# Optimization experiments

Measured on AMD Instinct MI355X. Metric: run time of the kernel, lower is better.

## Reference

```python
import jax, jax.numpy as jnp
import numpy as np

NH = 16      # num_heads
D = 128      # head_dim
C = 64       # chunk_size
EPS = 1e-12  # F.normalize eps


def setup_inputs() -> dict:
    key = jax.random.key(0)
    ks = jax.random.split(key, 12)
    B, L, H = 4, 4096, 2048
    std = 0.02
    f32 = jnp.float32
    inp = {
        "hidden_states": jax.random.normal(ks[0], (B, L, H), f32),
        # torch nn.Linear weights are [out_features, in_features]
        "q_w": jax.random.normal(ks[1], (NH * D, H), f32) * std,
        "q_b": jnp.zeros((NH * D,), f32),
        "k_w": jax.random.normal(ks[2], (NH * D, H), f32) * std,
        "k_b": jnp.zeros((NH * D,), f32),
        "v_w": jax.random.normal(ks[3], (NH * D, H), f32) * std,
        "v_b": jnp.zeros((NH * D,), f32),
        "a_w": jax.random.normal(ks[4], (NH, H), f32) * std,
        "a_b": jnp.zeros((NH,), f32),
        "b_w": jax.random.normal(ks[5], (NH, H), f32) * std,
        "b_b": jnp.zeros((NH,), f32),
        "og_w": jax.random.normal(ks[6], (NH * D, H), f32) * std,  # no bias
        "o_w": jax.random.normal(ks[7], (H, NH * D), f32) * std,
        "o_b": jnp.zeros((H,), f32),
    }
    return inp


def _l2norm(x):
    n = jnp.linalg.norm(x, axis=-1, keepdims=True)
    return x / jnp.maximum(n, EPS)


def reference(hidden_states, q_w, q_b, k_w, k_b, v_w, v_b,
              a_w, a_b, b_w, b_b, og_w, o_w, o_b):
    B, L, H = hidden_states.shape
    nh, d, c = NH, D, C
    hs = hidden_states

    q = (hs @ q_w.T + q_b).reshape(B, L, nh, d)
    k = (hs @ k_w.T + k_b).reshape(B, L, nh, d)
    v = (hs @ v_w.T + v_b).reshape(B, L, nh, d)
    # alpha = sigmoid(hs @ a_w.T + a_b) is computed in the original module but
    # never affects the output (alpha_mean / log_alpha are dead code) -> omitted.
    beta = jax.nn.softplus(hs @ b_w.T + b_b)            # [B,L,nh]

    scale = float(d) ** 0.5
    qn = _l2norm(q / scale)                              # normalize makes /scale moot, kept faithful
    kn = _l2norm(k / scale)
    gv = beta[..., None] * v                             # [B,L,nh,d]

    nchunks = L // c

    def to_chunks(x):  # [B,L,nh,d] -> [B,nchunks,nh,c,d]
        return x.reshape(B, nchunks, c, nh, d).transpose(0, 1, 3, 2, 4)

    qc, kc, gvc = to_chunks(qn), to_chunks(kn), to_chunks(gv)

    attn = jnp.einsum('bnhid,bnhjd->bnhij', qc, kc)      # per-chunk QK^T
    pos = jnp.arange(c, dtype=jnp.float32)
    dist = jnp.clip(pos[None, :] - pos[:, None], 0.0, None)   # (j-i) clamped >=0
    decay = jnp.exp(-0.1 * dist)
    causal = pos[None, :] <= pos[:, None]                # keep j<=i, zero j>i
    mask = jnp.where(causal, decay, 0.0)                 # [c,c]
    out = jnp.einsum('bnhij,bnhjd->bnhid', attn * mask, gvc)

    out = out.transpose(0, 1, 3, 2, 4).reshape(B, L, nh * d)
    gate = jax.nn.silu(hs @ og_w.T)                      # output_gate has no bias
    out = out * gate
    return out @ o_w.T + o_b
```

## Files before the change

kernel.cpp:

```cpp
#include <hip/hip_runtime.h>


typedef __bf16 bf16x8 __attribute__((ext_vector_type(8)));
typedef float f32x4 __attribute__((ext_vector_type(4)));

typedef __attribute__((address_space(1))) const unsigned int g_u32;
typedef __attribute__((address_space(3))) unsigned int l_u32;

__device__ __forceinline__ void cp16(const unsigned short* g, unsigned short* l) {
  __builtin_amdgcn_global_load_lds((g_u32*)g, (l_u32*)l, 16, 0, 0);
}

__device__ __forceinline__ unsigned short f2bf(float x) {
  unsigned u = __builtin_bit_cast(unsigned, x);
  u += 0x7fffu + ((u >> 16) & 1u);
  return (unsigned short)(u >> 16);
}
__device__ __forceinline__ float bf2f(unsigned short h) {
  return __builtin_bit_cast(float, (unsigned)h << 16);
}
__device__ __forceinline__ unsigned pk2(float a, float b) {
  return (unsigned)f2bf(a) | ((unsigned)f2bf(b) << 16);
}

__global__ __launch_bounds__(256) void cvt_bf16(const float* __restrict__ in,
                                                unsigned short* __restrict__ out,
                                                int n) {
  int i = (blockIdx.x * 256 + threadIdx.x) * 8;
  if (i >= n) return;
  float4 f0 = *(const float4*)(in + i);
  float4 f1 = *(const float4*)(in + i + 4);
  uint4 u;
  u.x = pk2(f0.x, f0.y); u.y = pk2(f0.z, f0.w);
  u.z = pk2(f1.x, f1.y); u.w = pk2(f1.z, f1.w);
  *(uint4*)(out + i) = u;
}

__global__ __launch_bounds__(256) void build_bias(
    const float* __restrict__ qb, const float* __restrict__ kb,
    const float* __restrict__ vb, float* __restrict__ bias_cat) {
  int i = blockIdx.x * 256 + threadIdx.x;
  float v = 0.f;
  if (i < 2048) v = qb[i];
  else if (i < 4096) v = kb[i - 2048];
  else if (i < 6144) v = vb[i - 4096];
  bias_cat[i] = v;
}

__global__ __launch_bounds__(256) void beta_kernel(
    const float* __restrict__ hs, const float* __restrict__ bw,
    const float* __restrict__ bb, float* __restrict__ beta,
    unsigned short* __restrict__ hsb) {
  __shared__ float row[2048];
  __shared__ float part[16][17];
  const int m = blockIdx.x;
  const float* src = hs + (size_t)m * 2048;
  for (int i = threadIdx.x; i < 512; i += 256)
    ((float4*)row)[i] = ((const float4*)src)[i];
  __syncthreads();
  if (hsb) {
    int e = threadIdx.x * 8;
    uint4 u;
    u.x = pk2(row[e], row[e + 1]);     u.y = pk2(row[e + 2], row[e + 3]);
    u.z = pk2(row[e + 4], row[e + 5]); u.w = pk2(row[e + 6], row[e + 7]);
    *(uint4*)(hsb + (size_t)m * 2048 + e) = u;
  }
  const int h = threadIdx.x >> 4, j = threadIdx.x & 15;
  const float* w = bw + h * 2048;
  float s = 0.f;
  #pragma unroll 8
  for (int kk = 0; kk < 128; kk++) {
    int k = j + (kk << 4);
    s += row[k] * w[k];
  }
  part[h][j] = s;
  __syncthreads();
  if (threadIdx.x < 16) {
    int hh = threadIdx.x;
    float t = bb[hh];
    #pragma unroll
    for (int j2 = 0; j2 < 16; j2++) t += part[hh][j2];
    beta[(size_t)m * 16 + hh] = fmaxf(t, 0.f) + log1pf(__expf(-fabsf(t)));
  }
}

template <int EPI, int N, int K>
__global__ __launch_bounds__(512, 2) void gemm256(
    const unsigned short* __restrict__ A, const unsigned short* __restrict__ Bw,
    const float* __restrict__ bias, const float* __restrict__ beta,
    void* __restrict__ Cv) {
  constexpr int NT = K / 64;
  static_assert(NT >= 3, "pipeline needs >=3 K-steps");
  __shared__ __align__(16) unsigned short S[2 * 32768];
  const int tid = threadIdx.x;
  const int m0 = blockIdx.y * 256;
  const int n0 = blockIdx.x * 256;
  const int wid = tid >> 6, lane = tid & 63;
  const int wm = wid >> 2, wn = wid & 3;
  const int quad = lane >> 4, l16 = lane & 15;

  const int sidx = tid >> 3;
  const int sc = tid & 7;
  const int scol = ((sc ^ (sidx & 7)) << 3);
  const unsigned short* pA = A + (size_t)(m0 + sidx) * K + scol;
  const int rbx = ((sidx >> 5) << 6) + (sidx & 31);
  const unsigned short* pB = Bw + (size_t)(n0 + rbx) * K + scol;

  auto STG = [&](int roff , const unsigned short* src) {
    cp16(src, S + roff + tid * 8);
    cp16(src + (size_t)128 * K, S + roff + 4096 + tid * 8);
  };

  const int sig = l16 & 7;
  const int ck0 = ((quad ^ sig) << 4);
  const int ck1 = (((4 + quad) ^ sig) << 4);
  const int aro = (wm * 64 + l16) * 128;
  const int bro = (wn * 32 + l16) * 128;

  f32x4 acc[8][4] = {};
  bf16x8 aL[4][2], aH[4][2], bX[2][2], bY[2][2];

  STG(0,             pA);
  STG(8192,          pA + (size_t)64 * K);
  STG(16384,         pB);
  STG(24576,         pB + (size_t)32 * K);
  STG(32768,         pA + 64);
  STG(32768 + 16384, pB + 64);
  STG(32768 + 24576, pB + (size_t)32 * K + 64);
  asm volatile("s_waitcnt vmcnt(6)" ::: "memory");
  __builtin_amdgcn_s_barrier();

  for (int t = 0; t < NT; ++t) {
    const int cur = (t & 1) << 15;
    const int nxt = 32768 - cur;
    const char* B0 = (const char*)S + cur * 2;
    const int koff1 = (t + 1 < NT ? t + 1 : NT - 1) * 64;
    const int koff2 = (t + 2 < NT ? t + 2 : NT - 1) * 64;

    #pragma unroll
    for (int mi = 0; mi < 4; mi++) {
      aL[mi][0] = *(const bf16x8*)(B0 + aro + mi * 2048 + ck0);
      aL[mi][1] = *(const bf16x8*)(B0 + aro + mi * 2048 + ck1);
    }
    #pragma unroll
    for (int ni = 0; ni < 2; ni++) {
      bX[ni][0] = *(const bf16x8*)(B0 + 32768 + bro + ni * 2048 + ck0);
      bX[ni][1] = *(const bf16x8*)(B0 + 32768 + bro + ni * 2048 + ck1);
    }
    STG(nxt + 8192, pA + (size_t)64 * K + koff1);
    __builtin_amdgcn_s_barrier();
    __builtin_amdgcn_s_setprio(1);
    #pragma unroll
    for (int k = 0; k < 2; k++)
      #pragma unroll
      for (int mi = 0; mi < 4; mi++)
        #pragma unroll
        for (int ni = 0; ni < 2; ni++)
          acc[mi][ni] = __builtin_amdgcn_mfma_f32_16x16x32_bf16(
              aL[mi][k], bX[ni][k], acc[mi][ni], 0, 0, 0);
    __builtin_amdgcn_s_setprio(0);
    __builtin_amdgcn_s_barrier();

    #pragma unroll
    for (int ni = 0; ni < 2; ni++) {
      bY[ni][0] = *(const bf16x8*)(B0 + 49152 + bro + ni * 2048 + ck0);
      bY[ni][1] = *(const bf16x8*)(B0 + 49152 + bro + ni * 2048 + ck1);
    }
    STG(cur, pA + koff2);
    __builtin_amdgcn_s_barrier();
    __builtin_amdgcn_s_setprio(1);
    #pragma unroll
    for (int k = 0; k < 2; k++)
      #pragma unroll
      for (int mi = 0; mi < 4; mi++)
        #pragma unroll
        for (int ni = 0; ni < 2; ni++)
          acc[mi][2 + ni] = __builtin_amdgcn_mfma_f32_16x16x32_bf16(
              aL[mi][k], bY[ni][k], acc[mi][2 + ni], 0, 0, 0);
    __builtin_amdgcn_s_setprio(0);
    __builtin_amdgcn_s_barrier();

    #pragma unroll
    for (int mi = 0; mi < 4; mi++) {
      aH[mi][0] = *(const bf16x8*)(B0 + 16384 + aro + mi * 2048 + ck0);
      aH[mi][1] = *(const bf16x8*)(B0 + 16384 + aro + mi * 2048 + ck1);
    }
    STG(cur + 16384, pB + koff2);
    __builtin_amdgcn_s_barrier();
    __builtin_amdgcn_s_setprio(1);
    #pragma unroll
    for (int k = 0; k < 2; k++)
      #pragma unroll
      for (int mi = 0; mi < 4; mi++)
        #pragma unroll
        for (int ni = 0; ni < 2; ni++)
          acc[4 + mi][2 + ni] = __builtin_amdgcn_mfma_f32_16x16x32_bf16(
              aH[mi][k], bY[ni][k], acc[4 + mi][2 + ni], 0, 0, 0);
    __builtin_amdgcn_s_setprio(0);
    __builtin_amdgcn_s_barrier();

    STG(cur + 24576, pB + (size_t)32 * K + koff2);
    __builtin_amdgcn_s_setprio(1);
    #pragma unroll
    for (int k = 0; k < 2; k++)
      #pragma unroll
      for (int mi = 0; mi < 4; mi++)
        #pragma unroll
        for (int ni = 0; ni < 2; ni++)
          acc[4 + mi][ni] = __builtin_amdgcn_mfma_f32_16x16x32_bf16(
              aH[mi][k], bX[ni][k], acc[4 + mi][ni], 0, 0, 0);
    __builtin_amdgcn_s_setprio(0);
    asm volatile("s_waitcnt vmcnt(6)" ::: "memory");
    __builtin_amdgcn_s_barrier();
  }
  asm volatile("s_waitcnt vmcnt(0)" ::: "memory");

  if (EPI == 0) {
    const int mode = n0 >> 11;
    unsigned short* outp =
        (unsigned short*)Cv + (size_t)mode * ((size_t)16384 * 2048);
    const int head = ((n0 + wn * 64) >> 7) & 15;
    #pragma unroll
    for (int mi = 0; mi < 8; mi++) {
      #pragma unroll
      for (int r = 0; r < 4; r++) {
        const int row = m0 + wm * 128 + mi * 16 + quad * 4 + r;
        const float bsc = (mode == 2) ? beta[(size_t)row * 16 + head] : 1.f;
        #pragma unroll
        for (int ni = 0; ni < 4; ni++) {
          const int col = n0 + wn * 64 + ni * 16 + l16;
          float x = acc[mi][ni][r] + bias[col];
          if (mode == 2) x *= bsc;
          if (mode == 3) x = x / (1.f + __expf(-x));
          outp[(size_t)row * 2048 + (col & 2047)] = f2bf(x);
        }
      }
    }
  } else {
    #pragma unroll
    for (int mi = 0; mi < 8; mi++)
      #pragma unroll
      for (int r = 0; r < 4; r++) {
        const int row = m0 + wm * 128 + mi * 16 + quad * 4 + r;
        #pragma unroll
        for (int ni = 0; ni < 4; ni++) {
          const int col = n0 + wn * 64 + ni * 16 + l16;
          ((float*)Cv)[(size_t)row * N + col] = acc[mi][ni][r] + bias[col];
        }
      }
  }
}

constexpr int GLDW = 40;
template <int EPI, bool ABF16>
__global__ __launch_bounds__(256) void gemm_bt(
    const void* __restrict__ Av, const float* __restrict__ Bw,
    const float* __restrict__ bias, const float* __restrict__ beta,
    void* __restrict__ Cv, int M, int N, int K) {
  __shared__ unsigned short As[128 * GLDW];
  __shared__ unsigned short Bs[128 * GLDW];
  const int tid = threadIdx.x;
  const int m0 = blockIdx.y * 128;
  const int n0 = blockIdx.x * 128;
  const int wid = tid >> 6, lane = tid & 63;
  const int wm = wid >> 1, wn = wid & 1;
  const int quad = lane >> 4, l16 = lane & 15;
  const int srow = tid >> 1, skh = (tid & 1) << 4;

  f32x4 acc[4][4] = {};
  const float* Bg = Bw + (size_t)(n0 + srow) * K + skh;

  for (int kb = 0; kb < K; kb += 32) {
    if (ABF16) {
      const unsigned short* Ag =
          (const unsigned short*)Av + (size_t)(m0 + srow) * K + kb + skh;
      uint4 u0 = ((const uint4*)Ag)[0];
      uint4 u1 = ((const uint4*)Ag)[1];
      uint4* d = (uint4*)&As[srow * GLDW + skh];
      d[0] = u0; d[1] = u1;
    } else {
      const float* Ag = (const float*)Av + (size_t)(m0 + srow) * K + kb + skh;
      float4 f0 = ((const float4*)Ag)[0];
      float4 f1 = ((const float4*)Ag)[1];
      float4 f2 = ((const float4*)Ag)[2];
      float4 f3 = ((const float4*)Ag)[3];
      unsigned* d = (unsigned*)&As[srow * GLDW + skh];
      d[0] = pk2(f0.x, f0.y); d[1] = pk2(f0.z, f0.w);
      d[2] = pk2(f1.x, f1.y); d[3] = pk2(f1.z, f1.w);
      d[4] = pk2(f2.x, f2.y); d[5] = pk2(f2.z, f2.w);
      d[6] = pk2(f3.x, f3.y); d[7] = pk2(f3.z, f3.w);
    }
    {
      const float* Bgk = Bg + kb;
      float4 f0 = ((const float4*)Bgk)[0];
      float4 f1 = ((const float4*)Bgk)[1];
      float4 f2 = ((const float4*)Bgk)[2];
      float4 f3 = ((const float4*)Bgk)[3];
      unsigned* d = (unsigned*)&Bs[srow * GLDW + skh];
      d[0] = pk2(f0.x, f0.y); d[1] = pk2(f0.z, f0.w);
      d[2] = pk2(f1.x, f1.y); d[3] = pk2(f1.z, f1.w);
      d[4] = pk2(f2.x, f2.y); d[5] = pk2(f2.z, f2.w);
      d[6] = pk2(f3.x, f3.y); d[7] = pk2(f3.z, f3.w);
    }
    __syncthreads();
    bf16x8 af[4], bfr[4];
    #pragma unroll
    for (int mi = 0; mi < 4; mi++)
      af[mi] = *(const bf16x8*)&As[(wm * 64 + mi * 16 + l16) * GLDW + (quad << 3)];
    #pragma unroll
    for (int ni = 0; ni < 4; ni++)
      bfr[ni] = *(const bf16x8*)&Bs[(wn * 64 + ni * 16 + l16) * GLDW + (quad << 3)];
    #pragma unroll
    for (int mi = 0; mi < 4; mi++)
      #pragma unroll
      for (int ni = 0; ni < 4; ni++)
        acc[mi][ni] = __builtin_amdgcn_mfma_f32_16x16x32_bf16(
            af[mi], bfr[ni], acc[mi][ni], 0, 0, 0);
    __syncthreads();
  }

  #pragma unroll
  for (int mi = 0; mi < 4; mi++) {
    #pragma unroll
    for (int r = 0; r < 4; r++) {
      const int row = m0 + wm * 64 + mi * 16 + quad * 4 + r;
      float bsc = 1.f;
      if (EPI == 1) bsc = beta[(size_t)row * 16 + blockIdx.x];
      #pragma unroll
      for (int ni = 0; ni < 4; ni++) {
        const int col = n0 + wn * 64 + ni * 16 + l16;
        float x = acc[mi][ni][r];
        if (EPI != 2) x += bias[col];
        if (EPI == 1) x *= bsc;
        if (EPI == 2) x = x / (1.f + __expf(-x));
        if (EPI == 3)
          ((float*)Cv)[(size_t)row * N + col] = x;
        else
          ((unsigned short*)Cv)[(size_t)row * N + col] = f2bf(x);
      }
    }
  }
}

constexpr int QK_LDW = 132;
constexpr int GT_LDW = 66;
constexpr int SS_LDW = 68;

__global__ __launch_bounds__(256) void attn_kernel(
    const unsigned short* __restrict__ qn, const unsigned short* __restrict__ kn,
    const unsigned short* __restrict__ gvp, const unsigned short* __restrict__ gate,
    unsigned short* __restrict__ y) {
  __shared__ unsigned short qs[64 * QK_LDW];
  __shared__ unsigned short ks[64 * QK_LDW];
  __shared__ unsigned short gst[128 * GT_LDW];
  __shared__ unsigned short Ss[64 * SS_LDW];

  const int tid = threadIdx.x;
  const int m0 = blockIdx.x * 64;
  const int h = blockIdx.y;
  const size_t gbase = (size_t)m0 * 2048 + (size_t)h * 128;

  #pragma unroll
  for (int it = 0; it < 4; it++) {
    int e = tid + it * 256;
    int i = e >> 4;
    int c = (e & 15) << 3;
    size_t g = gbase + (size_t)i * 2048 + c;
    *(uint4*)&qs[i * QK_LDW + c] = *(const uint4*)&qn[g];
    *(uint4*)&ks[i * QK_LDW + c] = *(const uint4*)&kn[g];
    uint4 gvv = *(const uint4*)&gvp[g];
    unsigned short tmp[8];
    *(uint4*)tmp = gvv;
    #pragma unroll
    for (int t = 0; t < 8; t++) gst[(c + t) * GT_LDW + i] = tmp[t];
  }
  __syncthreads();

  {
    const int rr = tid >> 2;
    const int seg = (tid & 3) * 32;
    float ssq = 0.f, ssk = 0.f;
    #pragma unroll
    for (int k2 = 0; k2 < 32; k2 += 2) {
      unsigned uq = *(const unsigned*)&qs[rr * QK_LDW + seg + k2];
      unsigned uk = *(const unsigned*)&ks[rr * QK_LDW + seg + k2];
      float a = bf2f((unsigned short)(uq & 0xffff)), b = bf2f((unsigned short)(uq >> 16));
      float c2 = bf2f((unsigned short)(uk & 0xffff)), d2 = bf2f((unsigned short)(uk >> 16));
      ssq += a * a + b * b;
      ssk += c2 * c2 + d2 * d2;
    }
    ssq += __shfl_xor(ssq, 1); ssq += __shfl_xor(ssq, 2);
    ssk += __shfl_xor(ssk, 1); ssk += __shfl_xor(ssk, 2);
    float iq = rsqrtf(fmaxf(ssq, 1e-24f));
    float ik = rsqrtf(fmaxf(ssk, 1e-24f));
    #pragma unroll
    for (int k2 = 0; k2 < 32; k2 += 2) {
      unsigned uq = *(const unsigned*)&qs[rr * QK_LDW + seg + k2];
      unsigned uk = *(const unsigned*)&ks[rr * QK_LDW + seg + k2];
      float a = bf2f((unsigned short)(uq & 0xffff)), b = bf2f((unsigned short)(uq >> 16));
      float c2 = bf2f((unsigned short)(uk & 0xffff)), d2 = bf2f((unsigned short)(uk >> 16));
      *(unsigned*)&qs[rr * QK_LDW + seg + k2] = pk2(a * iq, b * iq);
      *(unsigned*)&ks[rr * QK_LDW + seg + k2] = pk2(c2 * ik, d2 * ik);
    }
  }
  __syncthreads();

  const int w = tid >> 6;
  const int lane = tid & 63;
  const int quad = lane >> 4, l16 = lane & 15;

  {
    f32x4 acc[4] = {};
    #pragma unroll
    for (int kst = 0; kst < 4; kst++) {
      bf16x8 a = *(const bf16x8*)&qs[(w * 16 + l16) * QK_LDW + kst * 32 + (quad << 3)];
      #pragma unroll
      for (int ni = 0; ni < 4; ni++) {
        bf16x8 b = *(const bf16x8*)&ks[(ni * 16 + l16) * QK_LDW + kst * 32 + (quad << 3)];
        acc[ni] = __builtin_amdgcn_mfma_f32_16x16x32_bf16(a, b, acc[ni], 0, 0, 0);
      }
    }
    #pragma unroll
    for (int ni = 0; ni < 4; ni++)
      #pragma unroll
      for (int r = 0; r < 4; r++) {
        int row = w * 16 + quad * 4 + r;
        int col = ni * 16 + l16;
        float val = (col <= row) ? acc[ni][r] : 0.f;
        Ss[row * SS_LDW + col] = f2bf(val);
      }
  }
  __syncthreads();

  {
    f32x4 acc[8] = {};
    #pragma unroll
    for (int kst = 0; kst < 2; kst++) {
      bf16x8 a = *(const bf16x8*)&Ss[(w * 16 + l16) * SS_LDW + kst * 32 + (quad << 3)];
      #pragma unroll
      for (int nd = 0; nd < 8; nd++) {
        bf16x8 b = *(const bf16x8*)&gst[(nd * 16 + l16) * GT_LDW + kst * 32 + (quad << 3)];
        acc[nd] = __builtin_amdgcn_mfma_f32_16x16x32_bf16(a, b, acc[nd], 0, 0, 0);
      }
    }
    #pragma unroll
    for (int nd = 0; nd < 8; nd++)
      #pragma unroll
      for (int r = 0; r < 4; r++) {
        int row = w * 16 + quad * 4 + r;
        int col = nd * 16 + l16;
        size_t g = gbase + (size_t)row * 2048 + col;
        float gt = bf2f(gate[g]);
        y[g] = f2bf(acc[nd][r] * gt);
      }
  }
}

extern "C" void kernel_launch(void* const* d_in, const int* in_sizes, int n_in,
                              void* d_out, int out_size, void* d_ws, size_t ws_size,
                              hipStream_t stream) {
  const float* hs   = (const float*)d_in[0];
  const float* q_w  = (const float*)d_in[1];
  const float* q_b  = (const float*)d_in[2];
  const float* k_w  = (const float*)d_in[3];
  const float* k_b  = (const float*)d_in[4];
  const float* v_w  = (const float*)d_in[5];
  const float* v_b  = (const float*)d_in[6];
  const float* b_w  = (const float*)d_in[9];
  const float* b_b  = (const float*)d_in[10];
  const float* og_w = (const float*)d_in[11];
  const float* o_w  = (const float*)d_in[12];
  const float* o_b  = (const float*)d_in[13];

  const int M = 16384, K = 2048;
  const size_t MB64 = 67108864;

  const size_t OFF_HSB  = 4 * MB64;
  const size_t OFF_WCAT = OFF_HSB + MB64;
  const size_t OFF_OWB  = OFF_WCAT + 33554432;
  const size_t OFF_BETA = OFF_OWB + 8388608;
  const size_t OFF_BIAS = OFF_BETA + 1048576;
  const size_t NEED     = OFF_BIAS + 32768;

  char* ws = (char*)d_ws;

  if (ws_size >= NEED) {
    unsigned short* qy   = (unsigned short*)ws;
    unsigned short* knb  = (unsigned short*)(ws + MB64);
    unsigned short* gv   = (unsigned short*)(ws + 2 * MB64);
    unsigned short* gate = (unsigned short*)(ws + 3 * MB64);
    unsigned short* hsb  = (unsigned short*)(ws + OFF_HSB);
    unsigned short* wcat = (unsigned short*)(ws + OFF_WCAT);
    unsigned short* owb  = (unsigned short*)(ws + OFF_OWB);
    float*          beta = (float*)(ws + OFF_BETA);
    float*          bias = (float*)(ws + OFF_BIAS);

    const int NW = 4194304;
    cvt_bf16<<<NW / 2048, 256, 0, stream>>>(q_w,  wcat,          NW);
    cvt_bf16<<<NW / 2048, 256, 0, stream>>>(k_w,  wcat + NW,     NW);
    cvt_bf16<<<NW / 2048, 256, 0, stream>>>(v_w,  wcat + 2 * NW, NW);
    cvt_bf16<<<NW / 2048, 256, 0, stream>>>(og_w, wcat + 3 * NW, NW);
    cvt_bf16<<<NW / 2048, 256, 0, stream>>>(o_w,  owb,           NW);
    build_bias<<<32, 256, 0, stream>>>(q_b, k_b, v_b, bias);
    beta_kernel<<<M, 256, 0, stream>>>(hs, b_w, b_b, beta, hsb);

    gemm256<0, 8192, 2048><<<dim3(32, 64), 512, 0, stream>>>(
        hsb, wcat, bias, beta, qy);

    attn_kernel<<<dim3(256, 16), 256, 0, stream>>>(qy, knb, gv, gate, qy);

    gemm256<3, 2048, 2048><<<dim3(8, 64), 512, 0, stream>>>(
        qy, owb, o_b, nullptr, (float*)d_out);
  } else {
    unsigned short* qy   = (unsigned short*)ws;
    unsigned short* knb  = (unsigned short*)(ws + MB64);
    unsigned short* gv   = (unsigned short*)(ws + 2 * MB64);
    unsigned short* gate = (unsigned short*)(ws + 3 * MB64);
    float*          beta = (float*)(ws + 4 * MB64);

    beta_kernel<<<M, 256, 0, stream>>>(hs, b_w, b_b, beta, nullptr);
    dim3 gg(16, 128);
    gemm_bt<0, false><<<gg, 256, 0, stream>>>(hs, q_w, q_b, nullptr, qy, M, 2048, K);
    gemm_bt<0, false><<<gg, 256, 0, stream>>>(hs, k_w, k_b, nullptr, knb, M, 2048, K);
    gemm_bt<1, false><<<gg, 256, 0, stream>>>(hs, v_w, v_b, beta, gv, M, 2048, K);
    gemm_bt<2, false><<<gg, 256, 0, stream>>>(hs, og_w, nullptr, nullptr, gate, M, 2048, K);
    attn_kernel<<<dim3(256, 16), 256, 0, stream>>>(qy, knb, gv, gate, qy);
    gemm_bt<3, true><<<gg, 256, 0, stream>>>(qy, o_w, o_b, nullptr, (float*)d_out, M, 2048, K);
  }
}
```

Baseline: 1.137 ms.

## Switch gemm256 to 32x32x16 MFMA tiles and restructure K-loop pipeline

Replaces the 16x16x32 bf16 MFMA tiling in the main 256x256 GEMM with 32x32x16 MFMA instructions, so each wave holds 4x2 f32x16 accumulators instead of 8x4 f32x4. The K loop now walks four 16-wide k-slices with double-buffered fragment registers and uses one LDS wait plus barrier per step in place of four phase barriers. All global-to-LDS stages for step t+2 are issued after the last MFMA group. The epilogue is rewritten for the 32x32 output layout. The aim is fewer LDS fragment reads and fewer barriers per MFMA, at the cost of less interleaving between global loads and math.

New measurement: 1.447 ms. 27.2% more time.

```diff
diff --git a/kernel.cpp b/kernel.cpp
--- a/kernel.cpp
+++ b/kernel.cpp
@@ -3,6 +3,7 @@
 
 typedef __bf16 bf16x8 __attribute__((ext_vector_type(8)));
 typedef float f32x4 __attribute__((ext_vector_type(4)));
+typedef float f32x16 __attribute__((ext_vector_type(16)));
 
 typedef __attribute__((address_space(1))) const unsigned int g_u32;
 typedef __attribute__((address_space(3))) unsigned int l_u32;
@@ -97,7 +98,7 @@
   const int n0 = blockIdx.x * 256;
   const int wid = tid >> 6, lane = tid & 63;
   const int wm = wid >> 2, wn = wid & 3;
-  const int quad = lane >> 4, l16 = lane & 15;
+  const int l31 = lane & 31, kh = lane >> 5;
 
   const int sidx = tid >> 3;
   const int sc = tid & 7;
@@ -111,14 +112,21 @@
     cp16(src + (size_t)128 * K, S + roff + 4096 + tid * 8);
   };
 
-  const int sig = l16 & 7;
-  const int ck0 = ((quad ^ sig) << 4);
-  const int ck1 = (((4 + quad) ^ sig) << 4);
-  const int aro = (wm * 64 + l16) * 128;
-  const int bro = (wn * 32 + l16) * 128;
-
-  f32x4 acc[8][4] = {};
-  bf16x8 aL[4][2], aH[4][2], bX[2][2], bY[2][2];
+  const int sig = l31 & 7;
+  int Abase[4], Bbase[2];
+  #pragma unroll
+  for (int mt = 0; mt < 4; mt++)
+    Abase[mt] = ((mt < 2) ? 0 : 16384) + (wm * 64 + (mt & 1) * 32 + l31) * 128;
+  #pragma unroll
+  for (int nt = 0; nt < 2; nt++)
+    Bbase[nt] = 32768 + nt * 16384 + (wn * 32 + l31) * 128;
+  const int pf0 = (((0 * 2 + kh) ^ sig) << 4);
+  const int pf1 = (((1 * 2 + kh) ^ sig) << 4);
+  const int pf2 = (((2 * 2 + kh) ^ sig) << 4);
+  const int pf3 = (((3 * 2 + kh) ^ sig) << 4);
+
+  f32x16 acc[4][2] = {};
+  bf16x8 fa0[4], fb0[2], fa1[4], fb1[2];
 
   STG(0,             pA);
   STG(8192,          pA + (size_t)64 * K);
@@ -129,6 +137,7 @@
   STG(32768 + 24576, pB + (size_t)32 * K + 64);
   asm volatile("s_waitcnt vmcnt(6)" ::: "memory");
   __builtin_amdgcn_s_barrier();
+  __builtin_amdgcn_sched_barrier(0);
 
   for (int t = 0; t < NT; ++t) {
     const int cur = (t & 1) << 15;
@@ -138,80 +147,72 @@
     const int koff2 = (t + 2 < NT ? t + 2 : NT - 1) * 64;
 
     #pragma unroll
-    for (int mi = 0; mi < 4; mi++) {
-      aL[mi][0] = *(const bf16x8*)(B0 + aro + mi * 2048 + ck0);
-      aL[mi][1] = *(const bf16x8*)(B0 + aro + mi * 2048 + ck1);
-    }
-    #pragma unroll
-    for (int ni = 0; ni < 2; ni++) {
-      bX[ni][0] = *(const bf16x8*)(B0 + 32768 + bro + ni * 2048 + ck0);
-      bX[ni][1] = *(const bf16x8*)(B0 + 32768 + bro + ni * 2048 + ck1);
-    }
+    for (int mt = 0; mt < 4; mt++) fa0[mt] = *(const bf16x8*)(B0 + Abase[mt] + pf0);
+    #pragma unroll
+    for (int nt = 0; nt < 2; nt++) fb0[nt] = *(const bf16x8*)(B0 + Bbase[nt] + pf0);
+    #pragma unroll
+    for (int mt = 0; mt < 4; mt++) fa1[mt] = *(const bf16x8*)(B0 + Abase[mt] + pf1);
+    #pragma unroll
+    for (int nt = 0; nt < 2; nt++) fb1[nt] = *(const bf16x8*)(B0 + Bbase[nt] + pf1);
     STG(nxt + 8192, pA + (size_t)64 * K + koff1);
+
+    __builtin_amdgcn_s_setprio(1);
+    #pragma unroll
+    for (int mt = 0; mt < 4; mt++)
+      #pragma unroll
+      for (int nt = 0; nt < 2; nt++)
+        acc[mt][nt] = __builtin_amdgcn_mfma_f32_32x32x16_bf16(
+            fa0[mt], fb0[nt], acc[mt][nt], 0, 0, 0);
+    __builtin_amdgcn_s_setprio(0);
+
+    #pragma unroll
+    for (int mt = 0; mt < 4; mt++) fa0[mt] = *(const bf16x8*)(B0 + Abase[mt] + pf2);
+    #pragma unroll
+    for (int nt = 0; nt < 2; nt++) fb0[nt] = *(const bf16x8*)(B0 + Bbase[nt] + pf2);
+
+    __builtin_amdgcn_s_setprio(1);
+    #pragma unroll
+    for (int mt = 0; mt < 4; mt++)
+      #pragma unroll
+      for (int nt = 0; nt < 2; nt++)
+        acc[mt][nt] = __builtin_amdgcn_mfma_f32_32x32x16_bf16(
+            fa1[mt], fb1[nt], acc[mt][nt], 0, 0, 0);
+    __builtin_amdgcn_s_setprio(0);
+
+    #pragma unroll
+    for (int mt = 0; mt < 4; mt++) fa1[mt] = *(const bf16x8*)(B0 + Abase[mt] + pf3);
+    #pragma unroll
+    for (int nt = 0; nt < 2; nt++) fb1[nt] = *(const bf16x8*)(B0 + Bbase[nt] + pf3);
+
+    __builtin_amdgcn_s_setprio(1);
+    #pragma unroll
+    for (int mt = 0; mt < 4; mt++)
+      #pragma unroll
+      for (int nt = 0; nt < 2; nt++)
+        acc[mt][nt] = __builtin_amdgcn_mfma_f32_32x32x16_bf16(
+            fa0[mt], fb0[nt], acc[mt][nt], 0, 0, 0);
+    __builtin_amdgcn_s_setprio(0);
+
+    asm volatile("s_waitcnt lgkmcnt(0)" ::: "memory");
     __builtin_amdgcn_s_barrier();
+    __builtin_amdgcn_sched_barrier(0);
+
     __builtin_amdgcn_s_setprio(1);
     #pragma unroll
-    for (int k = 0; k < 2; k++)
-      #pragma unroll
-      for (int mi = 0; mi < 4; mi++)
-        #pragma unroll
-        for (int ni = 0; ni < 2; ni++)
-          acc[mi][ni] = __builtin_amdgcn_mfma_f32_16x16x32_bf16(
-              aL[mi][k], bX[ni][k], acc[mi][ni], 0, 0, 0);
+    for (int mt = 0; mt < 4; mt++)
+      #pragma unroll
+      for (int nt = 0; nt < 2; nt++)
+        acc[mt][nt] = __builtin_amdgcn_mfma_f32_32x32x16_bf16(
+            fa1[mt], fb1[nt], acc[mt][nt], 0, 0, 0);
     __builtin_amdgcn_s_setprio(0);
-    __builtin_amdgcn_s_barrier();
-
-    #pragma unroll
-    for (int ni = 0; ni < 2; ni++) {
-      bY[ni][0] = *(const bf16x8*)(B0 + 49152 + bro + ni * 2048 + ck0);
-      bY[ni][1] = *(const bf16x8*)(B0 + 49152 + bro + ni * 2048 + ck1);
-    }
-    STG(cur, pA + koff2);
-    __builtin_amdgcn_s_barrier();
-    __builtin_amdgcn_s_setprio(1);
-    #pragma unroll
-    for (int k = 0; k < 2; k++)
-      #pragma unroll
-      for (int mi = 0; mi < 4; mi++)
-        #pragma unroll
-        for (int ni = 0; ni < 2; ni++)
-          acc[mi][2 + ni] = __builtin_amdgcn_mfma_f32_16x16x32_bf16(
-              aL[mi][k], bY[ni][k], acc[mi][2 + ni], 0, 0, 0);
-    __builtin_amdgcn_s_setprio(0);
-    __builtin_amdgcn_s_barrier();
-
-    #pragma unroll
-    for (int mi = 0; mi < 4; mi++) {
-      aH[mi][0] = *(const bf16x8*)(B0 + 16384 + aro + mi * 2048 + ck0);
-      aH[mi][1] = *(const bf16x8*)(B0 + 16384 + aro + mi * 2048 + ck1);
-    }
+
+    STG(cur,         pA + koff2);
     STG(cur + 16384, pB + koff2);
-    __builtin_amdgcn_s_barrier();
-    __builtin_amdgcn_s_setprio(1);
-    #pragma unroll
-    for (int k = 0; k < 2; k++)
-      #pragma unroll
-      for (int mi = 0; mi < 4; mi++)
-        #pragma unroll
-        for (int ni = 0; ni < 2; ni++)
-          acc[4 + mi][2 + ni] = __builtin_amdgcn_mfma_f32_16x16x32_bf16(
-              aH[mi][k], bY[ni][k], acc[4 + mi][2 + ni], 0, 0, 0);
-    __builtin_amdgcn_s_setprio(0);
-    __builtin_amdgcn_s_barrier();
-
     STG(cur + 24576, pB + (size_t)32 * K + koff2);
-    __builtin_amdgcn_s_setprio(1);
-    #pragma unroll
-    for (int k = 0; k < 2; k++)
-      #pragma unroll
-      for (int mi = 0; mi < 4; mi++)
-        #pragma unroll
-        for (int ni = 0; ni < 2; ni++)
-          acc[4 + mi][ni] = __builtin_amdgcn_mfma_f32_16x16x32_bf16(
-              aH[mi][k], bX[ni][k], acc[4 + mi][ni], 0, 0, 0);
-    __builtin_amdgcn_s_setprio(0);
+
     asm volatile("s_waitcnt vmcnt(6)" ::: "memory");
     __builtin_amdgcn_s_barrier();
+    __builtin_amdgcn_sched_barrier(0);
   }
   asm volatile("s_waitcnt vmcnt(0)" ::: "memory");
 
@@ -219,35 +220,37 @@
     const int mode = n0 >> 11;
     unsigned short* outp =
         (unsigned short*)Cv + (size_t)mode * ((size_t)16384 * 2048);
-    const int head = ((n0 + wn * 64) >> 7) & 15;
-    #pragma unroll
-    for (int mi = 0; mi < 8; mi++) {
-      #pragma unroll
-      for (int r = 0; r < 4; r++) {
-        const int row = m0 + wm * 128 + mi * 16 + quad * 4 + r;
-        const float bsc = (mode == 2) ? beta[(size_t)row * 16 + head] : 1.f;
+    #pragma unroll
+    for (int nt = 0; nt < 2; nt++) {
+      const int colg = n0 + wn * 64 + nt * 32 + l31;
+      const int head = (colg >> 7) & 15;
+      const float bv = bias[colg];
+      #pragma unroll
+      for (int mt = 0; mt < 4; mt++) {
         #pragma unroll
-        for (int ni = 0; ni < 4; ni++) {
-          const int col = n0 + wn * 64 + ni * 16 + l16;
-          float x = acc[mi][ni][r] + bias[col];
-          if (mode == 2) x *= bsc;
+        for (int r = 0; r < 16; r++) {
+          const int row = m0 + wm * 128 + mt * 32 + (r & 3) + 8 * (r >> 2) + 4 * kh;
+          float x = acc[mt][nt][r] + bv;
+          if (mode == 2) x *= beta[(size_t)row * 16 + head];
           if (mode == 3) x = x / (1.f + __expf(-x));
-          outp[(size_t)row * 2048 + (col & 2047)] = f2bf(x);
+          outp[(size_t)row * 2048 + (colg & 2047)] = f2bf(x);
         }
       }
     }
   } else {
     #pragma unroll
-    for (int mi = 0; mi < 8; mi++)
-      #pragma unroll
-      for (int r = 0; r < 4; r++) {
-        const int row = m0 + wm * 128 + mi * 16 + quad * 4 + r;
+    for (int nt = 0; nt < 2; nt++) {
+      const int colg = n0 + wn * 64 + nt * 32 + l31;
+      const float bv = bias[colg];
+      #pragma unroll
+      for (int mt = 0; mt < 4; mt++) {
         #pragma unroll
-        for (int ni = 0; ni < 4; ni++) {
-          const int col = n0 + wn * 64 + ni * 16 + l16;
-          ((float*)Cv)[(size_t)row * N + col] = acc[mi][ni][r] + bias[col];
+        for (int r = 0; r < 16; r++) {
+          const int row = m0 + wm * 128 + mt * 32 + (r & 3) + 8 * (r >> 2) + 4 * kh;
+          ((float*)Cv)[(size_t)row * N + colg] = acc[mt][nt][r] + bv;
         }
       }
+    }
   }
 }
 
```
